# Kernel tuning notes

Hardware: AMD Instinct MI355X
Metric: run time of the kernel (lower is better)

## Reference

```python
import jax, jax.numpy as jnp
import numpy as np

H, C, HID, L, NF, B = 4, 128, 128, 3, 5, 32  # heads, per-head dim, hidden, layers, node feats, graphs
LN_EPS = 1e-5


def setup_inputs() -> dict:
    key = jax.random.key(0)
    ks = jax.random.split(key, 12)
    N, E = 10000, 160000
    x = jax.random.normal(ks[0], (N, NF), dtype=jnp.float32)
    edge_index = jax.random.randint(ks[1], (2, E), 0, N, dtype=jnp.int64)
    batch = jnp.sort(jax.random.randint(ks[2], (N,), 0, B, dtype=jnp.int64))
    s = 0.1
    return {
        "x": x,
        "edge_index": edge_index,
        "batch": batch,
        "node_W": jax.random.normal(ks[3], (NF, HID), dtype=jnp.float32) * s,
        "node_b": jnp.zeros((HID,), dtype=jnp.float32),
        "Ws": jax.random.normal(ks[4], (L, HID, H * C), dtype=jnp.float32) * s,
        "att_srcs": jax.random.normal(ks[5], (L, H, C), dtype=jnp.float32) * s,
        "att_dsts": jax.random.normal(ks[6], (L, H, C), dtype=jnp.float32) * s,
        "biases": jnp.zeros((L, HID), dtype=jnp.float32),
        "ln_gs": jnp.ones((L, HID), dtype=jnp.float32),
        "ln_bs": jnp.zeros((L, HID), dtype=jnp.float32),
    }


def _layer_norm(x, g, b):
    mu = jnp.mean(x, axis=-1, keepdims=True)
    var = jnp.mean(jnp.square(x - mu), axis=-1, keepdims=True)
    return (x - mu) * jax.lax.rsqrt(var + LN_EPS) * g + b


def _gat_layer(x, W, att_src, att_dst, bias, src, dst, N):
    # x: [N, HID]; PyG GATConv, heads=H, concat=False (mean over heads)
    h = (x @ W).reshape(N, H, C)                       # [N,H,C]
    a_src = jnp.sum(h * att_src, axis=-1)              # [N,H]
    a_dst = jnp.sum(h * att_dst, axis=-1)              # [N,H]
    e = jax.nn.leaky_relu(a_src[src] + a_dst[dst], 0.2)  # [E,H]
    # edge-softmax over destination neighborhoods (numerically stable)
    m = jax.ops.segment_max(e, dst, num_segments=N)
    ex = jnp.exp(e - m[dst])
    denom = jax.ops.segment_sum(ex, dst, num_segments=N)
    alpha = ex / (denom[dst] + 1e-16)                  # [E,H]
    msg = h[src] * alpha[:, :, None]                   # [E,H,C]
    out = jax.ops.segment_sum(msg, dst, num_segments=N)  # [N,H,C]
    return out.mean(axis=1) + bias                     # concat=False -> head mean


def reference(x, edge_index, batch, node_W, node_b, Ws, att_srcs, att_dsts,
              biases, ln_gs, ln_bs):
    N = x.shape[0]
    loop = jnp.arange(N, dtype=edge_index.dtype)
    src = jnp.concatenate([edge_index[0], loop])       # PyG adds self-loops
    dst = jnp.concatenate([edge_index[1], loop])

    h = jax.nn.relu(x @ node_W + node_b)               # [N,HID]
    for l in range(L):
        h_new = _gat_layer(h, Ws[l], att_srcs[l], att_dsts[l], biases[l], src, dst, N)
        h_new = _layer_norm(h_new, ln_gs[l], ln_bs[l])
        h = jax.nn.relu(h_new) + h                     # residual; dropout is identity in eval

    # global mean pool over graphs
    sums = jax.ops.segment_sum(h, batch, num_segments=B)
    cnts = jax.ops.segment_sum(jnp.ones((N, 1), h.dtype), batch, num_segments=B)
    graph_emb = sums / jnp.maximum(cnts, 1.0)
    return h, graph_emb
```

## Files before the change

kernel.cpp:

```cpp
#include <hip/hip_runtime.h>
#include <math.h>

#define N_NODES 10000
#define N_EDGES 160000
#define E2 (N_EDGES + N_NODES)
#define HIDDEN 128
#define NHEAD 4
#define NB 32
#define LN_EPS 1e-5f

#define T_INPUT (N_NODES * HIDDEN)
#define T_HIST  (T_INPUT + N_EDGES)
#define T_CONV  (T_HIST + 3 * 512 * 128)
#define T_BOUND (T_CONV + N_NODES)
#define T_TOTAL T_BOUND

typedef __attribute__((ext_vector_type(8))) short bf16x8;
typedef __attribute__((ext_vector_type(4))) float f32x4;

__device__ __forceinline__ unsigned short f2bf(float f) {
    unsigned int u = __float_as_uint(f);
    u += 0x7fffu + ((u >> 16) & 1u);
    return (unsigned short)(u >> 16);
}
__device__ __forceinline__ float bf2f_lo(unsigned int u) { return __uint_as_float(u << 16); }
__device__ __forceinline__ float bf2f_hi(unsigned int u) { return __uint_as_float(u & 0xffff0000u); }

__global__ __launch_bounds__(256) void k_pre(const float* __restrict__ x,
                                             const float* __restrict__ W,
                                             const float* __restrict__ b,
                                             const int* __restrict__ ei,
                                             const int* __restrict__ batch,
                                             const float* __restrict__ Ws,
                                             float* __restrict__ h,
                                             unsigned short* __restrict__ hb,
                                             int* counts, int* gstart, int* gend,
                                             unsigned short* __restrict__ Btb) {
    int t = blockIdx.x * blockDim.x + threadIdx.x;
    if (t < T_INPUT) {
        int n = t >> 7, c = t & 127;
        float s = b[c];
        #pragma unroll
        for (int k = 0; k < 5; k++) s += x[n * 5 + k] * W[k * HIDDEN + c];
        float r = fmaxf(s, 0.f);
        h[t] = r;
        hb[t] = f2bf(r);
    } else if (t < T_HIST) {
        int e = t - T_INPUT;
        atomicAdd(&counts[ei[N_EDGES + e]], 1);
    } else if (t < T_CONV) {
        int i = t - T_HIST;
        int l = i >> 16, rem = i & 65535;
        int n = rem >> 7, k = rem & 127;
        Btb[i] = f2bf(Ws[l * 65536 + k * 512 + n]);
    } else if (t < T_BOUND) {
        int n = t - T_CONV;
        int bb = batch[n];
        if (n == 0 || batch[n - 1] != bb) gstart[bb] = n;
        if (n == N_NODES - 1 || batch[n + 1] != bb) gend[bb] = n + 1;
    }
}

__global__ void k_scan(const int* __restrict__ counts, int* rowptr, int* cursor) {
    __shared__ int sums[1024];
    int t = threadIdx.x;
    const int per = 10;
    int base = t * per;
    int loc[per];
    int s = 0;
    for (int i = 0; i < per; i++) {
        int idx = base + i;
        int v = (idx < N_NODES) ? counts[idx] + 1 : 0;
        loc[i] = s; s += v;
    }
    sums[t] = s;
    __syncthreads();
    for (int off = 1; off < 1024; off <<= 1) {
        int v = (t >= off) ? sums[t - off] : 0;
        __syncthreads();
        sums[t] += v;
        __syncthreads();
    }
    int prefix = (t > 0) ? sums[t - 1] : 0;
    for (int i = 0; i < per; i++) {
        int idx = base + i;
        if (idx < N_NODES) { int r = prefix + loc[i]; rowptr[idx] = r; cursor[idx] = r; }
    }
    if (t == 1023) rowptr[N_NODES] = sums[1023];
}

__global__ void k_scatter(const int* __restrict__ ei, int* cursor, int* csr_src) {
    int e = blockIdx.x * blockDim.x + threadIdx.x;
    if (e < N_EDGES) {
        int s = ei[e], d = ei[N_EDGES + e];
        int pos = atomicAdd(&cursor[d], 1);
        csr_src[pos] = s;
    } else if (e < E2) {
        int n = e - N_EDGES;
        int pos = atomicAdd(&cursor[n], 1);
        csr_src[pos] = n;
    }
}

__global__ __launch_bounds__(256) void k_gemm_att(const unsigned short* __restrict__ Ab,
                                                  const unsigned short* __restrict__ Bt,
                                                  const float* __restrict__ ws,
                                                  const float* __restrict__ wd,
                                                  unsigned short* __restrict__ Cb,
                                                  float* __restrict__ a_src,
                                                  float* __restrict__ a_dst) {
    int wave = threadIdx.x >> 6, lane = threadIdx.x & 63;
    int q = lane >> 4, u = lane & 15;
    int h = blockIdx.x;
    int rowgrp = wave & 1, colhalf = wave >> 1;
    int mbase = blockIdx.y * 32 + rowgrp * 16;
    int colbase = h * 128 + colhalf * 64;
    int arow = mbase + u;
    if (arow > N_NODES - 1) arow = N_NODES - 1;
    bf16x8 a[4];
    #pragma unroll
    for (int k0 = 0; k0 < 4; k0++)
        a[k0] = *(const bf16x8*)(Ab + (size_t)arow * 128 + k0 * 32 + q * 8);
    f32x4 acc[4];
    #pragma unroll
    for (int nb = 0; nb < 4; nb++) acc[nb] = (f32x4){0.f, 0.f, 0.f, 0.f};
    #pragma unroll
    for (int nb = 0; nb < 4; nb++) {
        const unsigned short* bp = Bt + (size_t)(colbase + nb * 16 + u) * 128 + q * 8;
        #pragma unroll
        for (int k0 = 0; k0 < 4; k0++) {
            bf16x8 bfr = *(const bf16x8*)(bp + k0 * 32);
            acc[nb] = __builtin_amdgcn_mfma_f32_16x16x32_bf16(a[k0], bfr, acc[nb], 0, 0, 0);
        }
    }
    #pragma unroll
    for (int nb = 0; nb < 4; nb++) {
        int col = colbase + nb * 16 + u;
        #pragma unroll
        for (int r = 0; r < 4; r++) {
            int row = mbase + q * 4 + r;
            if (row < N_NODES) Cb[(size_t)row * 512 + col] = f2bf(acc[nb][r]);
        }
    }
    float ps[4] = {}, pd[4] = {};
    #pragma unroll
    for (int nb = 0; nb < 4; nb++) {
        int cl = colhalf * 64 + nb * 16 + u;
        float wsv = ws[h * 128 + cl], wdv = wd[h * 128 + cl];
        #pragma unroll
        for (int r = 0; r < 4; r++) { ps[r] += acc[nb][r] * wsv; pd[r] += acc[nb][r] * wdv; }
    }
    #pragma unroll
    for (int d = 1; d < 16; d <<= 1) {
        #pragma unroll
        for (int r = 0; r < 4; r++) {
            ps[r] += __shfl_xor(ps[r], d);
            pd[r] += __shfl_xor(pd[r], d);
        }
    }
    __shared__ float ls[2][2][16], ldd[2][2][16];
    if (u == 0) {
        #pragma unroll
        for (int r = 0; r < 4; r++) {
            ls[rowgrp][colhalf][q * 4 + r] = ps[r];
            ldd[rowgrp][colhalf][q * 4 + r] = pd[r];
        }
    }
    __syncthreads();
    if (colhalf == 0 && lane < 16) {
        int row = mbase + lane;
        if (row < N_NODES) {
            a_src[row * 4 + h] = ls[rowgrp][0][lane] + ls[rowgrp][1][lane];
            a_dst[row * 4 + h] = ldd[rowgrp][0][lane] + ldd[rowgrp][1][lane];
        }
    }
}

__global__ __launch_bounds__(256) void k_agg(const uint4* __restrict__ hb4,
                                             const int* __restrict__ rowptr,
                                             const int* __restrict__ csr,
                                             const float* __restrict__ a_src,
                                             const float* __restrict__ a_dst,
                                             const float* __restrict__ bias,
                                             const float* __restrict__ lng,
                                             const float* __restrict__ lnb,
                                             float* __restrict__ h,
                                             unsigned short* __restrict__ hbn) {
    int wave = threadIdx.x >> 6;
    int lane = threadIdx.x & 63;
    int n = blockIdx.x * 4 + wave;
    if (n >= N_NODES) return;
    int hl = lane >> 4;
    int pos = lane & 15;
    int off = rowptr[n];
    int deg = rowptr[n + 1] - off;
    float adn = a_dst[n * 4 + hl];
    float m = -INFINITY, denom = 0.f;
    float o[8] = {};
    for (int base = 0; base < deg; base += 64) {
        int cnt = min(64, deg - base);
        int s = (lane < cnt) ? csr[off + base + lane] : 0;
        for (int i = 0; i < cnt; i++) {
            int si = __shfl(s, i);
            float t = a_src[si * 4 + hl] + adn;
            float e = t > 0.f ? t : 0.2f * t;
            float nm = fmaxf(m, e);
            float sc = __expf(m - nm);
            float p = __expf(e - nm);
            denom = denom * sc + p;
            uint4 u = hb4[(size_t)si * 64 + lane];
            o[0] = o[0] * sc + p * bf2f_lo(u.x);
            o[1] = o[1] * sc + p * bf2f_hi(u.x);
            o[2] = o[2] * sc + p * bf2f_lo(u.y);
            o[3] = o[3] * sc + p * bf2f_hi(u.y);
            o[4] = o[4] * sc + p * bf2f_lo(u.z);
            o[5] = o[5] * sc + p * bf2f_hi(u.z);
            o[6] = o[6] * sc + p * bf2f_lo(u.w);
            o[7] = o[7] * sc + p * bf2f_hi(u.w);
            m = nm;
        }
    }
    float inv = 1.f / (denom + 1e-16f);
    #pragma unroll
    for (int k = 0; k < 8; k++) o[k] *= inv;
    #pragma unroll
    for (int k = 0; k < 8; k++) {
        o[k] += __shfl_xor(o[k], 16);
        o[k] += __shfl_xor(o[k], 32);
    }
    float v[8], sv = 0.f, sq = 0.f;
    #pragma unroll
    for (int k = 0; k < 8; k++) {
        float b = bias[8 * pos + k];
        v[k] = 0.25f * o[k] + b;
        sv += v[k]; sq += v[k] * v[k];
    }
    #pragma unroll
    for (int d = 8; d > 0; d >>= 1) {
        sv += __shfl_xor(sv, d);
        sq += __shfl_xor(sq, d);
    }
    float mu = sv * (1.f / 128.f);
    float var = sq * (1.f / 128.f) - mu * mu;
    float rs = rsqrtf(var + LN_EPS);
    if (hl == 0) {
        float* hrow = h + (size_t)n * 128 + 8 * pos;
        float4 old0 = *(const float4*)(hrow);
        float4 old1 = *(const float4*)(hrow + 4);
        float r[8];
        #pragma unroll
        for (int k = 0; k < 8; k++) {
            float y = (v[k] - mu) * rs * lng[8 * pos + k] + lnb[8 * pos + k];
            r[k] = fmaxf(y, 0.f);
        }
        float w[8] = {r[0] + old0.x, r[1] + old0.y, r[2] + old0.z, r[3] + old0.w,
                      r[4] + old1.x, r[5] + old1.y, r[6] + old1.z, r[7] + old1.w};
        *(float4*)(hrow) = make_float4(w[0], w[1], w[2], w[3]);
        *(float4*)(hrow + 4) = make_float4(w[4], w[5], w[6], w[7]);
        ushort4 p0, p1;
        p0.x = f2bf(w[0]); p0.y = f2bf(w[1]); p0.z = f2bf(w[2]); p0.w = f2bf(w[3]);
        p1.x = f2bf(w[4]); p1.y = f2bf(w[5]); p1.z = f2bf(w[6]); p1.w = f2bf(w[7]);
        unsigned short* hbrow = hbn + (size_t)n * 128 + 8 * pos;
        *(ushort4*)(hbrow) = p0;
        *(ushort4*)(hbrow + 4) = p1;
    }
}

#define POOL_CHUNK 32
__global__ __launch_bounds__(128) void k_pool_sum(const float* __restrict__ h,
                                                  const int* __restrict__ batch,
                                                  const int* __restrict__ gstart,
                                                  const int* __restrict__ gend,
                                                  float* __restrict__ gout) {
    int n0 = blockIdx.x * POOL_CHUNK;
    int c = threadIdx.x;
    int nend = min(n0 + POOL_CHUNK, N_NODES);
    if (n0 >= N_NODES) return;
    int cur = batch[n0];
    float acc = 0.f;
    for (int n = n0; n < nend; n++) {
        int b = batch[n];
        if (b != cur) {
            float inv = 1.f / (float)max(gend[cur] - gstart[cur], 1);
            atomicAdd(&gout[cur * HIDDEN + c], acc * inv);
            acc = 0.f; cur = b;
        }
        acc += h[(size_t)n * HIDDEN + c];
    }
    float inv = 1.f / (float)max(gend[cur] - gstart[cur], 1);
    atomicAdd(&gout[cur * HIDDEN + c], acc * inv);
}

extern "C" void kernel_launch(void* const* d_in, const int* in_sizes, int n_in,
                              void* d_out, int out_size, void* d_ws, size_t ws_size,
                              hipStream_t stream) {
    const float* x      = (const float*)d_in[0];
    const int*   ei     = (const int*)d_in[1];
    const int*   batch  = (const int*)d_in[2];
    const float* node_W = (const float*)d_in[3];
    const float* node_b = (const float*)d_in[4];
    const float* Ws     = (const float*)d_in[5];
    const float* att_s  = (const float*)d_in[6];
    const float* att_d  = (const float*)d_in[7];
    const float* biases = (const float*)d_in[8];
    const float* ln_g   = (const float*)d_in[9];
    const float* ln_b   = (const float*)d_in[10];

    float* out = (float*)d_out;
    float* h = out;
    float* gout = out + (size_t)N_NODES * HIDDEN;

    char* w = (char*)d_ws;
    auto carve = [&](size_t bytes) {
        void* p = (void*)w;
        w += (bytes + 255) & ~(size_t)255;
        return p;
    };
    int* rowptr  = (int*)carve((N_NODES + 1) * sizeof(int));
    int* cursor  = (int*)carve(N_NODES * sizeof(int));
    int* counts  = (int*)carve(N_NODES * sizeof(int));
    int* csr     = (int*)carve(E2 * sizeof(int));
    int* gstart  = (int*)carve(NB * sizeof(int));
    int* gend    = (int*)carve(NB * sizeof(int));
    float* a_src = (float*)carve((size_t)N_NODES * NHEAD * sizeof(float));
    float* a_dst = (float*)carve((size_t)N_NODES * NHEAD * sizeof(float));
    unsigned short* hb  = (unsigned short*)carve((size_t)N_NODES * 512 * sizeof(unsigned short));
    unsigned short* hbx = (unsigned short*)carve((size_t)N_NODES * HIDDEN * sizeof(unsigned short));
    unsigned short* Btb = (unsigned short*)carve((size_t)3 * 512 * 128 * sizeof(unsigned short));

    hipMemsetAsync(counts, 0, N_NODES * sizeof(int), stream);
    hipMemsetAsync(gout, 0, NB * HIDDEN * sizeof(float), stream);

    k_pre<<<(T_TOTAL + 255) / 256, 256, 0, stream>>>(x, node_W, node_b, ei, batch, Ws,
                                                     h, hbx, counts, gstart, gend, Btb);
    k_scan<<<1, 1024, 0, stream>>>(counts, rowptr, cursor);
    k_scatter<<<(E2 + 255) / 256, 256, 0, stream>>>(ei, cursor, csr);

    for (int l = 0; l < 3; l++) {
        k_gemm_att<<<dim3(4, (N_NODES + 31) / 32), 256, 0, stream>>>(
            hbx, Btb + (size_t)l * 512 * 128,
            att_s + l * NHEAD * 128, att_d + l * NHEAD * 128,
            hb, a_src, a_dst);
        k_agg<<<(N_NODES + 3) / 4, 256, 0, stream>>>((const uint4*)hb, rowptr, csr,
                                           a_src, a_dst,
                                           biases + l * HIDDEN, ln_g + l * HIDDEN,
                                           ln_b + l * HIDDEN, h, hbx);
    }
    k_pool_sum<<<(N_NODES + POOL_CHUNK - 1) / POOL_CHUNK, 128, 0, stream>>>(
        h, batch, gstart, gend, gout);
}
```

Before: 272.6 us.

## Unroll edge aggregation by 4 with padded CSR and fuse pooling into last layer

CSR row starts are padded to multiples of 4 so each wave can load four neighbor indices with one int4 read and issue four independent row gathers per iteration. This raises memory-level parallelism in the online softmax aggregation, with one rescale per group of four edges. The global mean pool kernel is removed: the last layer's aggregation atomically adds each node's scaled output into the graph embedding and skips the unneeded bf16 write. The cost is many more atomics (one per element per node) and a slightly larger CSR buffer.

```diff
diff --git a/kernel.cpp b/kernel.cpp
--- a/kernel.cpp
+++ b/kernel.cpp
@@ -25,6 +25,7 @@
 }
 __device__ __forceinline__ float bf2f_lo(unsigned int u) { return __uint_as_float(u << 16); }
 __device__ __forceinline__ float bf2f_hi(unsigned int u) { return __uint_as_float(u & 0xffff0000u); }
+__device__ __forceinline__ float lrelu(float t) { return t > 0.f ? t : 0.2f * t; }
 
 __global__ __launch_bounds__(256) void k_pre(const float* __restrict__ x,
                                              const float* __restrict__ W,
@@ -70,7 +71,7 @@
     int s = 0;
     for (int i = 0; i < per; i++) {
         int idx = base + i;
-        int v = (idx < N_NODES) ? counts[idx] + 1 : 0;
+        int v = (idx < N_NODES) ? ((counts[idx] + 1 + 3) & ~3) : 0;
         loc[i] = s; s += v;
     }
     sums[t] = s;
@@ -178,6 +179,7 @@
 
 __global__ __launch_bounds__(256) void k_agg(const uint4* __restrict__ hb4,
                                              const int* __restrict__ rowptr,
+                                             const int* __restrict__ counts,
                                              const int* __restrict__ csr,
                                              const float* __restrict__ a_src,
                                              const float* __restrict__ a_dst,
@@ -185,7 +187,12 @@
                                              const float* __restrict__ lng,
                                              const float* __restrict__ lnb,
                                              float* __restrict__ h,
-                                             unsigned short* __restrict__ hbn) {
+                                             unsigned short* __restrict__ hbn,
+                                             const int* __restrict__ batch,
+                                             const int* __restrict__ gstart,
+                                             const int* __restrict__ gend,
+                                             float* __restrict__ gout,
+                                             int last) {
     int wave = threadIdx.x >> 6;
     int lane = threadIdx.x & 63;
     int n = blockIdx.x * 4 + wave;
@@ -193,32 +200,41 @@
     int hl = lane >> 4;
     int pos = lane & 15;
     int off = rowptr[n];
-    int deg = rowptr[n + 1] - off;
+    int deg = counts[n] + 1;
     float adn = a_dst[n * 4 + hl];
     float m = -INFINITY, denom = 0.f;
     float o[8] = {};
-    for (int base = 0; base < deg; base += 64) {
-        int cnt = min(64, deg - base);
-        int s = (lane < cnt) ? csr[off + base + lane] : 0;
-        for (int i = 0; i < cnt; i++) {
-            int si = __shfl(s, i);
-            float t = a_src[si * 4 + hl] + adn;
-            float e = t > 0.f ? t : 0.2f * t;
-            float nm = fmaxf(m, e);
-            float sc = __expf(m - nm);
-            float p = __expf(e - nm);
-            denom = denom * sc + p;
-            uint4 u = hb4[(size_t)si * 64 + lane];
-            o[0] = o[0] * sc + p * bf2f_lo(u.x);
-            o[1] = o[1] * sc + p * bf2f_hi(u.x);
-            o[2] = o[2] * sc + p * bf2f_lo(u.y);
-            o[3] = o[3] * sc + p * bf2f_hi(u.y);
-            o[4] = o[4] * sc + p * bf2f_lo(u.z);
-            o[5] = o[5] * sc + p * bf2f_hi(u.z);
-            o[6] = o[6] * sc + p * bf2f_lo(u.w);
-            o[7] = o[7] * sc + p * bf2f_hi(u.w);
-            m = nm;
-        }
+    for (int i = 0; i < deg; i += 4) {
+        int4 s4 = *(const int4*)(csr + off + i);
+        int rem = deg - i;
+        int s0 = s4.x;
+        int s1 = (rem > 1) ? s4.y : s0;
+        int s2 = (rem > 2) ? s4.z : s0;
+        int s3 = (rem > 3) ? s4.w : s0;
+        uint4 u0 = hb4[(size_t)s0 * 64 + lane];
+        uint4 u1 = hb4[(size_t)s1 * 64 + lane];
+        uint4 u2 = hb4[(size_t)s2 * 64 + lane];
+        uint4 u3 = hb4[(size_t)s3 * 64 + lane];
+        float e0 = lrelu(a_src[s0 * 4 + hl] + adn);
+        float e1 = (rem > 1) ? lrelu(a_src[s1 * 4 + hl] + adn) : -INFINITY;
+        float e2 = (rem > 2) ? lrelu(a_src[s2 * 4 + hl] + adn) : -INFINITY;
+        float e3 = (rem > 3) ? lrelu(a_src[s3 * 4 + hl] + adn) : -INFINITY;
+        float nm = fmaxf(fmaxf(fmaxf(e0, e1), fmaxf(e2, e3)), m);
+        float sc = __expf(m - nm);
+        float p0 = __expf(e0 - nm);
+        float p1 = __expf(e1 - nm);
+        float p2 = __expf(e2 - nm);
+        float p3 = __expf(e3 - nm);
+        denom = denom * sc + ((p0 + p1) + (p2 + p3));
+        o[0] = o[0] * sc + p0 * bf2f_lo(u0.x) + p1 * bf2f_lo(u1.x) + p2 * bf2f_lo(u2.x) + p3 * bf2f_lo(u3.x);
+        o[1] = o[1] * sc + p0 * bf2f_hi(u0.x) + p1 * bf2f_hi(u1.x) + p2 * bf2f_hi(u2.x) + p3 * bf2f_hi(u3.x);
+        o[2] = o[2] * sc + p0 * bf2f_lo(u0.y) + p1 * bf2f_lo(u1.y) + p2 * bf2f_lo(u2.y) + p3 * bf2f_lo(u3.y);
+        o[3] = o[3] * sc + p0 * bf2f_hi(u0.y) + p1 * bf2f_hi(u1.y) + p2 * bf2f_hi(u2.y) + p3 * bf2f_hi(u3.y);
+        o[4] = o[4] * sc + p0 * bf2f_lo(u0.z) + p1 * bf2f_lo(u1.z) + p2 * bf2f_lo(u2.z) + p3 * bf2f_lo(u3.z);
+        o[5] = o[5] * sc + p0 * bf2f_hi(u0.z) + p1 * bf2f_hi(u1.z) + p2 * bf2f_hi(u2.z) + p3 * bf2f_hi(u3.z);
+        o[6] = o[6] * sc + p0 * bf2f_lo(u0.w) + p1 * bf2f_lo(u1.w) + p2 * bf2f_lo(u2.w) + p3 * bf2f_lo(u3.w);
+        o[7] = o[7] * sc + p0 * bf2f_hi(u0.w) + p1 * bf2f_hi(u1.w) + p2 * bf2f_hi(u2.w) + p3 * bf2f_hi(u3.w);
+        m = nm;
     }
     float inv = 1.f / (denom + 1e-16f);
     #pragma unroll
@@ -257,38 +273,21 @@
                       r[4] + old1.x, r[5] + old1.y, r[6] + old1.z, r[7] + old1.w};
         *(float4*)(hrow) = make_float4(w[0], w[1], w[2], w[3]);
         *(float4*)(hrow + 4) = make_float4(w[4], w[5], w[6], w[7]);
-        ushort4 p0, p1;
-        p0.x = f2bf(w[0]); p0.y = f2bf(w[1]); p0.z = f2bf(w[2]); p0.w = f2bf(w[3]);
-        p1.x = f2bf(w[4]); p1.y = f2bf(w[5]); p1.z = f2bf(w[6]); p1.w = f2bf(w[7]);
-        unsigned short* hbrow = hbn + (size_t)n * 128 + 8 * pos;
-        *(ushort4*)(hbrow) = p0;
-        *(ushort4*)(hbrow + 4) = p1;
-    }
-}
-
-#define POOL_CHUNK 32
-__global__ __launch_bounds__(128) void k_pool_sum(const float* __restrict__ h,
-                                                  const int* __restrict__ batch,
-                                                  const int* __restrict__ gstart,
-                                                  const int* __restrict__ gend,
-                                                  float* __restrict__ gout) {
-    int n0 = blockIdx.x * POOL_CHUNK;
-    int c = threadIdx.x;
-    int nend = min(n0 + POOL_CHUNK, N_NODES);
-    if (n0 >= N_NODES) return;
-    int cur = batch[n0];
-    float acc = 0.f;
-    for (int n = n0; n < nend; n++) {
-        int b = batch[n];
-        if (b != cur) {
-            float inv = 1.f / (float)max(gend[cur] - gstart[cur], 1);
-            atomicAdd(&gout[cur * HIDDEN + c], acc * inv);
-            acc = 0.f; cur = b;
-        }
-        acc += h[(size_t)n * HIDDEN + c];
-    }
-    float inv = 1.f / (float)max(gend[cur] - gstart[cur], 1);
-    atomicAdd(&gout[cur * HIDDEN + c], acc * inv);
+        if (last) {
+            int b = batch[n];
+            float invc = 1.f / (float)max(gend[b] - gstart[b], 1);
+            #pragma unroll
+            for (int k = 0; k < 8; k++)
+                atomicAdd(&gout[b * 128 + 8 * pos + k], w[k] * invc);
+        } else {
+            ushort4 p0, p1;
+            p0.x = f2bf(w[0]); p0.y = f2bf(w[1]); p0.z = f2bf(w[2]); p0.w = f2bf(w[3]);
+            p1.x = f2bf(w[4]); p1.y = f2bf(w[5]); p1.z = f2bf(w[6]); p1.w = f2bf(w[7]);
+            unsigned short* hbrow = hbn + (size_t)n * 128 + 8 * pos;
+            *(ushort4*)(hbrow) = p0;
+            *(ushort4*)(hbrow + 4) = p1;
+        }
+    }
 }
 
 extern "C" void kernel_launch(void* const* d_in, const int* in_sizes, int n_in,
@@ -319,7 +318,7 @@
     int* rowptr  = (int*)carve((N_NODES + 1) * sizeof(int));
     int* cursor  = (int*)carve(N_NODES * sizeof(int));
     int* counts  = (int*)carve(N_NODES * sizeof(int));
-    int* csr     = (int*)carve(E2 * sizeof(int));
+    int* csr     = (int*)carve((E2 + 4 * N_NODES + 16) * sizeof(int));
     int* gstart  = (int*)carve(NB * sizeof(int));
     int* gend    = (int*)carve(NB * sizeof(int));
     float* a_src = (float*)carve((size_t)N_NODES * NHEAD * sizeof(float));
@@ -341,11 +340,10 @@
             hbx, Btb + (size_t)l * 512 * 128,
             att_s + l * NHEAD * 128, att_d + l * NHEAD * 128,
             hb, a_src, a_dst);
-        k_agg<<<(N_NODES + 3) / 4, 256, 0, stream>>>((const uint4*)hb, rowptr, csr,
+        k_agg<<<(N_NODES + 3) / 4, 256, 0, stream>>>((const uint4*)hb, rowptr, counts, csr,
                                            a_src, a_dst,
                                            biases + l * HIDDEN, ln_g + l * HIDDEN,
-                                           ln_b + l * HIDDEN, h, hbx);
-    }
-    k_pool_sum<<<(N_NODES + POOL_CHUNK - 1) / POOL_CHUNK, 128, 0, stream>>>(
-        h, batch, gstart, gend, gout);
-}
+                                           ln_b + l * HIDDEN, h, hbx,
+                                           batch, gstart, gend, gout, (l == 2) ? 1 : 0);
+    }
+}
```

Result: slower. 374.4 us (+37.4%).
